# Kernel optimization log

Measured on AMD Instinct MI355X. Metric: run time of the kernel, lower is better.

## Reference

```python
import jax, jax.numpy as jnp
import numpy as np

D_MODEL = 1024
H = 16
DK = D_MODEL // H
D_FC = 4096
B = 2
S = 1024
EPS = 1e-6


def setup_inputs() -> dict:
    key = jax.random.key(0)
    ks = jax.random.split(key, 8)
    sc = 1.0 / np.sqrt(D_MODEL)
    return {
        "x": jax.random.normal(ks[0], (B, S, D_MODEL), dtype=jnp.float32),
        "mask": jnp.ones((B, 1, 1, S), dtype=jnp.int32),
        "w_q": jax.random.normal(ks[1], (D_MODEL, D_MODEL), dtype=jnp.float32) * sc,
        "w_k": jax.random.normal(ks[2], (D_MODEL, D_MODEL), dtype=jnp.float32) * sc,
        "w_v": jax.random.normal(ks[3], (D_MODEL, D_MODEL), dtype=jnp.float32) * sc,
        "w_o": jax.random.normal(ks[4], (D_MODEL, D_MODEL), dtype=jnp.float32) * sc,
        "alpha1": jnp.ones((D_MODEL,), dtype=jnp.float32),
        "beta1": jnp.zeros((D_MODEL,), dtype=jnp.float32),
        "alpha2": jnp.ones((D_MODEL,), dtype=jnp.float32),
        "beta2": jnp.zeros((D_MODEL,), dtype=jnp.float32),
        "fc1_w": jax.random.normal(ks[5], (D_FC, D_MODEL), dtype=jnp.float32) * sc,
        "fc1_b": jnp.zeros((D_FC,), dtype=jnp.float32),
        "fc2_w": jax.random.normal(ks[6], (D_MODEL, D_FC), dtype=jnp.float32) * (1.0 / np.sqrt(D_FC)),
        "fc2_b": jnp.zeros((D_MODEL,), dtype=jnp.float32),
    }


def _layernorm(x, alpha, beta):
    # Matches torch: mean and std (unbiased, ddof=1), divide by (std + eps)
    mean = jnp.mean(x, axis=-1, keepdims=True)
    std = jnp.std(x, axis=-1, keepdims=True, ddof=1)
    return alpha * (x - mean) / (std + EPS) + beta


def _mha(x, mask, w_q, w_k, w_v, w_o):
    # nn.Linear(bias=False): y = x @ W.T
    q = (x @ w_q.T).reshape(B, S, H, DK).transpose(0, 2, 1, 3)  # (B,H,S,DK)
    k = (x @ w_k.T).reshape(B, S, H, DK).transpose(0, 2, 1, 3)
    v = (x @ w_v.T).reshape(B, S, H, DK).transpose(0, 2, 1, 3)
    scores = jnp.einsum('bhqd,bhkd->bhqk', q, k) / jnp.sqrt(jnp.float32(DK))
    scores = jnp.where(mask == 0, jnp.float32(-1e9), scores)
    attn = jax.nn.softmax(scores, axis=-1)  # dropout=0 (eval)
    out = jnp.einsum('bhqk,bhkd->bhqd', attn, v)  # (B,H,S,DK)
    out = out.transpose(0, 2, 1, 3).reshape(B, S, D_MODEL)
    return out @ w_o.T


def _ffn(x, fc1_w, fc1_b, fc2_w, fc2_b):
    h = jax.nn.relu(x @ fc1_w.T + fc1_b)
    return h @ fc2_w.T + fc2_b


def reference(x, mask, w_q, w_k, w_v, w_o, alpha1, beta1, alpha2, beta2,
              fc1_w, fc1_b, fc2_w, fc2_b):
    # Pre-LN residual block 1: attention
    x = x + _mha(_layernorm(x, alpha1, beta1), mask, w_q, w_k, w_v, w_o)
    # Pre-LN residual block 2: FFN
    x = x + _ffn(_layernorm(x, alpha2, beta2), fc1_w, fc1_b, fc2_w, fc2_b)
    return x
```

## Files before the change

kernel.cpp:

```cpp
#include <hip/hip_runtime.h>
#include <hip/hip_bf16.h>


typedef __bf16 bf16;
typedef __attribute__((ext_vector_type(8))) __bf16 bf16x8;
typedef __attribute__((ext_vector_type(4))) __bf16 bf16x4;
typedef __attribute__((ext_vector_type(4))) float f32x4;

#define NTOK 2048
#define DM   1024
#define DFC  4096
#define QKVN 3072

__device__ inline void gl_lds16(const void* g, void* l) {
    __builtin_amdgcn_global_load_lds((const __attribute__((address_space(1))) void*)g,
                                     (__attribute__((address_space(3))) void*)l, 16, 0, 0);
}

__device__ inline void ln_row(float4 v, const float* alpha, const float* beta,
                              bf16* outrow, int t) {
    float s  = v.x + v.y + v.z + v.w;
    float ss = v.x * v.x + v.y * v.y + v.z * v.z + v.w * v.w;
    __shared__ float red[8];
    int lane = t & 63, wv = t >> 6;
    #pragma unroll
    for (int o = 32; o > 0; o >>= 1) {
        s  += __shfl_down(s, o);
        ss += __shfl_down(ss, o);
    }
    if (lane == 0) { red[wv] = s; red[4 + wv] = ss; }
    __syncthreads();
    float S  = red[0] + red[1] + red[2] + red[3];
    float SS = red[4] + red[5] + red[6] + red[7];
    float mean = S * (1.0f / 1024.0f);
    float var  = (SS - S * mean) * (1.0f / 1023.0f);
    var = var < 0.f ? 0.f : var;
    float inv = 1.0f / (sqrtf(var) + 1e-6f);
    float4 a4 = reinterpret_cast<const float4*>(alpha)[t];
    float4 b4 = reinterpret_cast<const float4*>(beta)[t];
    bf16x4 o4;
    o4[0] = (bf16)(a4.x * (v.x - mean) * inv + b4.x);
    o4[1] = (bf16)(a4.y * (v.y - mean) * inv + b4.y);
    o4[2] = (bf16)(a4.z * (v.z - mean) * inv + b4.z);
    o4[3] = (bf16)(a4.w * (v.w - mean) * inv + b4.w);
    reinterpret_cast<bf16x4*>(outrow)[t] = o4;
}

__global__ __launch_bounds__(256) void prep_kernel(
    const float4* __restrict__ wq, const float4* __restrict__ wk,
    const float4* __restrict__ wv, const float4* __restrict__ wo,
    const float4* __restrict__ f1, const float4* __restrict__ f2,
    bf16x4* __restrict__ oqkv, bf16x4* __restrict__ oo,
    bf16x4* __restrict__ of1, bf16x4* __restrict__ of2,
    const float* __restrict__ x, const float* __restrict__ alpha1,
    const float* __restrict__ beta1, bf16* __restrict__ xn) {
    int blk = blockIdx.x;
    int t = threadIdx.x;
    if (blk < 12288) {
        int i = blk * 256 + t;
        const int Q = 262144;
        float4 v;
        bf16x4* dst;
        if (i < 3 * Q) {
            v = (i < Q) ? wq[i] : (i < 2 * Q) ? wk[i - Q] : wv[i - 2 * Q];
            dst = oqkv + i;
        } else if (i < 4 * Q) {
            v = wo[i - 3 * Q];
            dst = oo + (i - 3 * Q);
        } else if (i < 8 * Q) {
            v = f1[i - 4 * Q];
            dst = of1 + (i - 4 * Q);
        } else {
            v = f2[i - 8 * Q];
            dst = of2 + (i - 8 * Q);
        }
        bf16x4 o;
        o[0] = (bf16)v.x; o[1] = (bf16)v.y; o[2] = (bf16)v.z; o[3] = (bf16)v.w;
        *dst = o;
    } else {
        int row = blk - 12288;
        float4 v = reinterpret_cast<const float4*>(x + (size_t)row * DM)[t];
        ln_row(v, alpha1, beta1, xn + (size_t)row * DM, t);
    }
}

__global__ __launch_bounds__(256) void reduce_ln_kernel(const float* __restrict__ p,
                                                        const float* __restrict__ resid,
                                                        const float* __restrict__ alpha,
                                                        const float* __restrict__ beta,
                                                        float* __restrict__ x2,
                                                        bf16* __restrict__ xn) {
    int row = blockIdx.x, t = threadIdx.x;
    size_t i4 = (size_t)row * 256 + t;
    const size_t SL = 524288;
    float4 a = reinterpret_cast<const float4*>(p)[i4];
    float4 b = reinterpret_cast<const float4*>(p)[i4 + SL];
    float4 c = reinterpret_cast<const float4*>(p)[i4 + 2 * SL];
    float4 d = reinterpret_cast<const float4*>(p)[i4 + 3 * SL];
    float4 r = reinterpret_cast<const float4*>(resid)[i4];
    float4 v;
    v.x = a.x + b.x + c.x + d.x + r.x;
    v.y = a.y + b.y + c.y + d.y + r.y;
    v.z = a.z + b.z + c.z + d.z + r.z;
    v.w = a.w + b.w + c.w + d.w + r.w;
    reinterpret_cast<float4*>(x2)[i4] = v;
    ln_row(v, alpha, beta, xn + (size_t)row * DM, t);
}

__global__ __launch_bounds__(256) void reduce_out_kernel(const float* __restrict__ p,
                                                         const float* __restrict__ bias,
                                                         const float* __restrict__ x2,
                                                         float* __restrict__ out) {
    size_t i4 = (size_t)blockIdx.x * 256 + threadIdx.x;
    const size_t SL = 524288;
    float4 a = reinterpret_cast<const float4*>(p)[i4];
    float4 b = reinterpret_cast<const float4*>(p)[i4 + SL];
    float4 c = reinterpret_cast<const float4*>(p)[i4 + 2 * SL];
    float4 d = reinterpret_cast<const float4*>(p)[i4 + 3 * SL];
    float4 r = reinterpret_cast<const float4*>(x2)[i4];
    float4 bi = reinterpret_cast<const float4*>(bias)[i4 & 255];
    float4 o;
    o.x = a.x + b.x + c.x + d.x + r.x + bi.x;
    o.y = a.y + b.y + c.y + d.y + r.y + bi.y;
    o.z = a.z + b.z + c.z + d.z + r.z + bi.z;
    o.w = a.w + b.w + c.w + d.w + r.w + bi.w;
    reinterpret_cast<float4*>(out)[i4] = o;
}

template <int EPI>
__global__ __launch_bounds__(256) void gemm128(const bf16* __restrict__ A,
                                               const bf16* __restrict__ Bt,
                                               void* __restrict__ outp,
                                               bf16* __restrict__ vt,
                                               const float* __restrict__ bias,
                                               int M, int N, int K, int kslice) {
    __shared__ bf16 As[2][128 * 64];
    __shared__ bf16 Bs[2][128 * 64];
    int tid = threadIdx.x;
    int lane = tid & 63, wave = tid >> 6;
    int q = lane >> 4, r = lane & 15;
    int wm = wave >> 1, wn = wave & 1;

    int lid = blockIdx.y * gridDim.x + blockIdx.x;
    int nxp = gridDim.x >> 3;
    int xcd = lid & 7;
    int loc = lid >> 3;
    int bx = xcd * nxp + (loc % nxp);
    int by = loc / nxp;

    int m0 = by * 128, n0 = bx * 128;
    int kbeg = blockIdx.z * kslice;
    int nit = kslice / 64;
    f32x4 acc[4][4] = {};

    int srow = tid >> 3;
    int csrc = (tid & 7) ^ (srow & 7);
    const bf16* agp = A  + (size_t)(m0 + srow) * K + kbeg + csrc * 8;
    const bf16* bgp = Bt + (size_t)(n0 + srow) * K + kbeg + csrc * 8;

    int rsw = (r & 7);
    int co0 = ((q ^ rsw) * 8);
    int co1 = co0 ^ 32;
    int aoff = (wm * 64 + r) * 64;
    int boff = (wn * 64 + r) * 64;

    auto stage = [&](int it, int b) {
        int k0 = it * 64;
        #pragma unroll
        for (int j = 0; j < 4; ++j) {
            gl_lds16(agp + (size_t)j * 32 * K + k0, &As[b][tid * 8 + j * 2048]);
            gl_lds16(bgp + (size_t)j * 32 * K + k0, &Bs[b][tid * 8 + j * 2048]);
        }
    };

    stage(0, 0);
    for (int it = 0; it < nit; ++it) {
        __syncthreads();
        if (it + 1 < nit) stage(it + 1, (it + 1) & 1);
        const bf16* Ab = &As[it & 1][aoff];
        const bf16* Bb = &Bs[it & 1][boff];
        #pragma unroll
        for (int half = 0; half < 2; ++half) {
            int co = half ? co1 : co0;
            bf16x8 af[4], bfv[4];
            #pragma unroll
            for (int t = 0; t < 4; ++t)
                af[t] = *reinterpret_cast<const bf16x8*>(Ab + t * 1024 + co);
            #pragma unroll
            for (int u = 0; u < 4; ++u)
                bfv[u] = *reinterpret_cast<const bf16x8*>(Bb + u * 1024 + co);
            #pragma unroll
            for (int t = 0; t < 4; ++t)
                #pragma unroll
                for (int u = 0; u < 4; ++u)
                    acc[t][u] = __builtin_amdgcn_mfma_f32_16x16x32_bf16(af[t], bfv[u], acc[t][u], 0, 0, 0);
        }
    }

    if (EPI == 2 && n0 >= 2048) {
        int bb = m0 >> 10;
        int sb = (m0 & 1023) + wm * 64 + q * 4;
        int vrow0 = bb * 1024 + (n0 - 2048) + wn * 64;
        #pragma unroll
        for (int t = 0; t < 4; ++t) {
            #pragma unroll
            for (int u = 0; u < 4; ++u) {
                bf16x4 pk;
                #pragma unroll
                for (int i = 0; i < 4; ++i) pk[i] = (bf16)acc[t][u][i];
                *reinterpret_cast<bf16x4*>(vt + (size_t)(vrow0 + u * 16 + r) * 1024 + sb + t * 16) = pk;
            }
        }
        return;
    }

    size_t zoff = (size_t)blockIdx.z * M * N;
    #pragma unroll
    for (int t = 0; t < 4; ++t) {
        #pragma unroll
        for (int u = 0; u < 4; ++u) {
            #pragma unroll
            for (int i = 0; i < 4; ++i) {
                int mm = m0 + wm * 64 + t * 16 + q * 4 + i;
                int nn = n0 + wn * 64 + u * 16 + r;
                size_t idx = (size_t)mm * N + nn;
                float v = acc[t][u][i];
                if (EPI == 0 || EPI == 2) {
                    ((bf16*)outp)[idx] = (bf16)v;
                } else if (EPI == 1) {
                    v += bias[nn];
                    ((bf16*)outp)[idx] = (bf16)(v > 0.f ? v : 0.f);
                } else {
                    ((float*)outp)[zoff + idx] = v;
                }
            }
        }
    }
}

__global__ __launch_bounds__(256) void attn_kernel(const bf16* __restrict__ qkv,
                                                   const bf16* __restrict__ Vt,
                                                   const int* __restrict__ mask,
                                                   bf16* __restrict__ out) {
    __shared__ bf16 Ks[2][4096];
    __shared__ bf16 Vs[2][4096];
    __shared__ bf16 pbuf[4][1024];
    __shared__ float msk[1024];
    int tid = threadIdx.x;
    int lane = tid & 63, w = tid >> 6;
    int q = lane >> 4, r = lane & 15;

    int id = blockIdx.x;
    int xcd = id & 7, j = id >> 3;
    int bh = xcd * 4 + (j >> 4);
    int qb = j & 15;
    int b = bh >> 4, h = bh & 15;

    {
        int4 mi = reinterpret_cast<const int4*>(mask + b * 1024)[tid];
        msk[tid * 4 + 0] = mi.x ? 0.f : -1e9f;
        msk[tid * 4 + 1] = mi.y ? 0.f : -1e9f;
        msk[tid * 4 + 2] = mi.z ? 0.f : -1e9f;
        msk[tid * 4 + 3] = mi.w ? 0.f : -1e9f;
    }

    const bf16* qrow = qkv + (size_t)(b * 1024 + qb * 64 + w * 16 + r) * QKVN + h * 64 + q * 8;
    bf16x8 qf0 = *reinterpret_cast<const bf16x8*>(qrow);
    bf16x8 qf1 = *reinterpret_cast<const bf16x8*>(qrow + 32);

    int csw = (tid & 7) ^ ((tid >> 3) & 7);
    const bf16* kg0 = qkv + (size_t)(b * 1024 + (tid >> 3)) * QKVN + 1024 + h * 64 + csw * 8;
    const bf16* kg1 = kg0 + (size_t)32 * QKVN;
    const bf16* vg0 = Vt + (size_t)((b * 16 + h) * 64 + (tid >> 3)) * 1024 + csw * 8;
    const bf16* vg1 = vg0 + 32 * 1024;
    bf16* kld = &Ks[0][tid * 8];
    bf16* vld = &Vs[0][tid * 8];

    int co0 = (q ^ (r & 7)) * 8;
    bf16* pw = pbuf[w];
    bf16x8 ones;
    #pragma unroll
    for (int jj = 0; jj < 8; ++jj) ones[jj] = (bf16)1.0f;

    float m[4] = {-1e30f, -1e30f, -1e30f, -1e30f};
    f32x4 osum = {};
    f32x4 o[4] = {};

    gl_lds16(kg0, kld);
    gl_lds16(kg1, kld + 2048);
    gl_lds16(vg0, vld);
    gl_lds16(vg1, vld + 2048);

    for (int t = 0; t < 16; ++t) {
        __syncthreads();
        if (t < 15) {
            int ktn = (t + 1) * 64;
            int bo = ((t + 1) & 1) * 4096;
            gl_lds16(kg0 + (size_t)ktn * QKVN, kld + bo);
            gl_lds16(kg1 + (size_t)ktn * QKVN, kld + bo + 2048);
            gl_lds16(vg0 + ktn, vld + bo);
            gl_lds16(vg1 + ktn, vld + bo + 2048);
        }
        const bf16* Kb = Ks[t & 1];
        const bf16* Vb = Vs[t & 1];
        int kt = t * 64;

        f32x4 s[4];
        #pragma unroll
        for (int ks = 0; ks < 4; ++ks) {
            bf16x8 kf0 = *reinterpret_cast<const bf16x8*>(&Kb[(ks * 16 + r) * 64 + co0]);
            bf16x8 kf1 = *reinterpret_cast<const bf16x8*>(&Kb[(ks * 16 + r) * 64 + (co0 ^ 32)]);
            f32x4 a = {};
            a = __builtin_amdgcn_mfma_f32_16x16x32_bf16(qf0, kf0, a, 0, 0, 0);
            a = __builtin_amdgcn_mfma_f32_16x16x32_bf16(qf1, kf1, a, 0, 0, 0);
            float mb = msk[kt + ks * 16 + r];
            #pragma unroll
            for (int i = 0; i < 4; ++i) s[ks][i] = fmaf(a[i], 0.125f, mb);
        }
        float alpha[4];
        #pragma unroll
        for (int i = 0; i < 4; ++i) {
            float t2 = fmaxf(fmaxf(s[0][i], s[1][i]), fmaxf(s[2][i], s[3][i]));
            t2 = fmaxf(t2, __shfl_xor(t2, 1));
            t2 = fmaxf(t2, __shfl_xor(t2, 2));
            t2 = fmaxf(t2, __shfl_xor(t2, 4));
            t2 = fmaxf(t2, __shfl_xor(t2, 8));
            float mn = fmaxf(m[i], t2);
            alpha[i] = __expf(m[i] - mn);
            m[i] = mn;
        }
        #pragma unroll
        for (int i = 0; i < 4; ++i) {
            s[0][i] = __expf(s[0][i] - m[i]);
            s[1][i] = __expf(s[1][i] - m[i]);
            s[2][i] = __expf(s[2][i] - m[i]);
            s[3][i] = __expf(s[3][i] - m[i]);
        }
        #pragma unroll
        for (int i = 0; i < 4; ++i) {
            osum[i] *= alpha[i];
            o[0][i] *= alpha[i]; o[1][i] *= alpha[i];
            o[2][i] *= alpha[i]; o[3][i] *= alpha[i];
        }
        #pragma unroll
        for (int ks = 0; ks < 4; ++ks) {
            int kc = ks * 2 + (r >> 3);
            #pragma unroll
            for (int i = 0; i < 4; ++i) {
                int mr = q * 4 + i;
                pw[mr * 64 + ((kc ^ (mr & 7)) * 8) + (r & 7)] = (bf16)s[ks][i];
            }
        }
        #pragma unroll
        for (int ks2 = 0; ks2 < 2; ++ks2) {
            int vpo = (((ks2 * 4 + q) ^ (r & 7)) * 8);
            bf16x8 pf = *reinterpret_cast<const bf16x8*>(&pw[r * 64 + vpo]);
            #pragma unroll
            for (int nt = 0; nt < 4; ++nt) {
                bf16x8 vf = *reinterpret_cast<const bf16x8*>(&Vb[(nt * 16 + r) * 64 + vpo]);
                o[nt] = __builtin_amdgcn_mfma_f32_16x16x32_bf16(pf, vf, o[nt], 0, 0, 0);
            }
            osum = __builtin_amdgcn_mfma_f32_16x16x32_bf16(pf, ones, osum, 0, 0, 0);
        }
    }

    float inv[4];
    #pragma unroll
    for (int i = 0; i < 4; ++i) inv[i] = 1.0f / osum[i];
    #pragma unroll
    for (int nt = 0; nt < 4; ++nt)
        #pragma unroll
        for (int i = 0; i < 4; ++i)
            out[(size_t)(b * 1024 + qb * 64 + w * 16 + q * 4 + i) * DM + h * 64 + nt * 16 + r] =
                (bf16)(o[nt][i] * inv[i]);
}

extern "C" void kernel_launch(void* const* d_in, const int* in_sizes, int n_in,
                              void* d_out, int out_size, void* d_ws, size_t ws_size,
                              hipStream_t stream) {
    const float* x      = (const float*)d_in[0];
    const int*   mask   = (const int*)  d_in[1];
    const float* w_q    = (const float*)d_in[2];
    const float* w_k    = (const float*)d_in[3];
    const float* w_v    = (const float*)d_in[4];
    const float* w_o    = (const float*)d_in[5];
    const float* alpha1 = (const float*)d_in[6];
    const float* beta1  = (const float*)d_in[7];
    const float* alpha2 = (const float*)d_in[8];
    const float* beta2  = (const float*)d_in[9];
    const float* fc1_w  = (const float*)d_in[10];
    const float* fc1_b  = (const float*)d_in[11];
    const float* fc2_w  = (const float*)d_in[12];
    const float* fc2_b  = (const float*)d_in[13];
    float* out = (float*)d_out;

    char* ws = (char*)d_ws;
    const size_t MB = 1024 * 1024;
    bf16*  wqkv_b = (bf16*)(ws +  0 * MB);
    bf16*  wo_b   = (bf16*)(ws +  6 * MB);
    bf16*  f1w_b  = (bf16*)(ws +  8 * MB);
    bf16*  f2w_b  = (bf16*)(ws + 16 * MB);
    bf16*  xn     = (bf16*)(ws + 24 * MB);
    bf16*  qkvb   = (bf16*)(ws + 28 * MB);
    bf16*  vtb    = (bf16*)(ws + 40 * MB);
    bf16*  attnb  = (bf16*)(ws + 44 * MB);
    float* x2     = (float*)(ws + 48 * MB);
    float* po     = (float*)(ws + 56 * MB);
    bf16*  hb     = (bf16*)(ws + 28 * MB);
    float* pf2    = (float*)(ws + 56 * MB);

    prep_kernel<<<14336, 256, 0, stream>>>(
        (const float4*)w_q, (const float4*)w_k, (const float4*)w_v, (const float4*)w_o,
        (const float4*)fc1_w, (const float4*)fc2_w,
        (bf16x4*)wqkv_b, (bf16x4*)wo_b, (bf16x4*)f1w_b, (bf16x4*)f2w_b,
        x, alpha1, beta1, xn);

    gemm128<2><<<dim3(QKVN / 128, NTOK / 128, 1), 256, 0, stream>>>(
        xn, wqkv_b, qkvb, vtb, nullptr, NTOK, QKVN, DM, DM);

    attn_kernel<<<512, 256, 0, stream>>>(qkvb, vtb, mask, attnb);

    gemm128<4><<<dim3(DM / 128, NTOK / 128, 4), 256, 0, stream>>>(
        attnb, wo_b, po, nullptr, nullptr, NTOK, DM, DM, DM / 4);

    reduce_ln_kernel<<<NTOK, 256, 0, stream>>>(po, x, alpha2, beta2, x2, xn);

    gemm128<1><<<dim3(DFC / 128, NTOK / 128, 1), 256, 0, stream>>>(
        xn, f1w_b, hb, nullptr, fc1_b, NTOK, DFC, DM, DM);

    gemm128<4><<<dim3(DM / 128, NTOK / 128, 4), 256, 0, stream>>>(
        hb, f2w_b, pf2, nullptr, nullptr, NTOK, DM, DFC, DFC / 4);

    reduce_out_kernel<<<2048, 256, 0, stream>>>(pf2, fc2_b, x2, out);
}
```

Measured before the change: 252.2 us.

## Overlap weight conversion with QKV GEMM and replace split-K with 128x64 tiles

```diff
diff --git a/kernel.cpp b/kernel.cpp
--- a/kernel.cpp
+++ b/kernel.cpp
@@ -48,37 +48,20 @@
 
 __global__ __launch_bounds__(256) void prep_kernel(
     const float4* __restrict__ wq, const float4* __restrict__ wk,
-    const float4* __restrict__ wv, const float4* __restrict__ wo,
-    const float4* __restrict__ f1, const float4* __restrict__ f2,
-    bf16x4* __restrict__ oqkv, bf16x4* __restrict__ oo,
-    bf16x4* __restrict__ of1, bf16x4* __restrict__ of2,
+    const float4* __restrict__ wv, bf16x4* __restrict__ oqkv,
     const float* __restrict__ x, const float* __restrict__ alpha1,
     const float* __restrict__ beta1, bf16* __restrict__ xn) {
     int blk = blockIdx.x;
     int t = threadIdx.x;
-    if (blk < 12288) {
+    if (blk < 3072) {
         int i = blk * 256 + t;
         const int Q = 262144;
-        float4 v;
-        bf16x4* dst;
-        if (i < 3 * Q) {
-            v = (i < Q) ? wq[i] : (i < 2 * Q) ? wk[i - Q] : wv[i - 2 * Q];
-            dst = oqkv + i;
-        } else if (i < 4 * Q) {
-            v = wo[i - 3 * Q];
-            dst = oo + (i - 3 * Q);
-        } else if (i < 8 * Q) {
-            v = f1[i - 4 * Q];
-            dst = of1 + (i - 4 * Q);
-        } else {
-            v = f2[i - 8 * Q];
-            dst = of2 + (i - 8 * Q);
-        }
+        float4 v = (i < Q) ? wq[i] : (i < 2 * Q) ? wk[i - Q] : wv[i - 2 * Q];
         bf16x4 o;
         o[0] = (bf16)v.x; o[1] = (bf16)v.y; o[2] = (bf16)v.z; o[3] = (bf16)v.w;
-        *dst = o;
+        oqkv[i] = o;
     } else {
-        int row = blk - 12288;
+        int row = blk - 3072;
         float4 v = reinterpret_cast<const float4*>(x + (size_t)row * DM)[t];
         ln_row(v, alpha1, beta1, xn + (size_t)row * DM, t);
     }
@@ -92,17 +75,10 @@
                                                         bf16* __restrict__ xn) {
     int row = blockIdx.x, t = threadIdx.x;
     size_t i4 = (size_t)row * 256 + t;
-    const size_t SL = 524288;
     float4 a = reinterpret_cast<const float4*>(p)[i4];
-    float4 b = reinterpret_cast<const float4*>(p)[i4 + SL];
-    float4 c = reinterpret_cast<const float4*>(p)[i4 + 2 * SL];
-    float4 d = reinterpret_cast<const float4*>(p)[i4 + 3 * SL];
     float4 r = reinterpret_cast<const float4*>(resid)[i4];
     float4 v;
-    v.x = a.x + b.x + c.x + d.x + r.x;
-    v.y = a.y + b.y + c.y + d.y + r.y;
-    v.z = a.z + b.z + c.z + d.z + r.z;
-    v.w = a.w + b.w + c.w + d.w + r.w;
+    v.x = a.x + r.x; v.y = a.y + r.y; v.z = a.z + r.z; v.w = a.w + r.w;
     reinterpret_cast<float4*>(x2)[i4] = v;
     ln_row(v, alpha, beta, xn + (size_t)row * DM, t);
 }
@@ -112,18 +88,12 @@
                                                          const float* __restrict__ x2,
                                                          float* __restrict__ out) {
     size_t i4 = (size_t)blockIdx.x * 256 + threadIdx.x;
-    const size_t SL = 524288;
     float4 a = reinterpret_cast<const float4*>(p)[i4];
-    float4 b = reinterpret_cast<const float4*>(p)[i4 + SL];
-    float4 c = reinterpret_cast<const float4*>(p)[i4 + 2 * SL];
-    float4 d = reinterpret_cast<const float4*>(p)[i4 + 3 * SL];
     float4 r = reinterpret_cast<const float4*>(x2)[i4];
     float4 bi = reinterpret_cast<const float4*>(bias)[i4 & 255];
     float4 o;
-    o.x = a.x + b.x + c.x + d.x + r.x + bi.x;
-    o.y = a.y + b.y + c.y + d.y + r.y + bi.y;
-    o.z = a.z + b.z + c.z + d.z + r.z + bi.z;
-    o.w = a.w + b.w + c.w + d.w + r.w + bi.w;
+    o.x = a.x + r.x + bi.x; o.y = a.y + r.y + bi.y;
+    o.z = a.z + r.z + bi.z; o.w = a.w + r.w + bi.w;
     reinterpret_cast<float4*>(out)[i4] = o;
 }
 
@@ -133,9 +103,141 @@
                                                void* __restrict__ outp,
                                                bf16* __restrict__ vt,
                                                const float* __restrict__ bias,
-                                               int M, int N, int K, int kslice) {
+                                               int M, int N, int K,
+                                               int nbx, int nby,
+                                               const float4* __restrict__ cwo,
+                                               const float4* __restrict__ cf1,
+                                               const float4* __restrict__ cf2,
+                                               bf16x4* __restrict__ oo,
+                                               bf16x4* __restrict__ of1,
+                                               bf16x4* __restrict__ of2) {
     __shared__ bf16 As[2][128 * 64];
     __shared__ bf16 Bs[2][128 * 64];
+    int tid = threadIdx.x;
+    int lid = blockIdx.y * nbx + blockIdx.x;
+
+    if (EPI == 2) {
+        if (lid >= nbx * nby) {
+            int i = (lid - nbx * nby) * 256 + tid;
+            const int Q = 262144;
+            float4 v;
+            bf16x4* dst;
+            if (i < Q) {
+                v = cwo[i];  dst = oo + i;
+            } else if (i < 5 * Q) {
+                v = cf1[i - Q]; dst = of1 + (i - Q);
+            } else {
+                v = cf2[i - 5 * Q]; dst = of2 + (i - 5 * Q);
+            }
+            bf16x4 o;
+            o[0] = (bf16)v.x; o[1] = (bf16)v.y; o[2] = (bf16)v.z; o[3] = (bf16)v.w;
+            *dst = o;
+            return;
+        }
+    }
+
+    int lane = tid & 63, wave = tid >> 6;
+    int q = lane >> 4, r = lane & 15;
+    int wm = wave >> 1, wn = wave & 1;
+
+    int nxp = nbx >> 3;
+    int xcd = lid & 7;
+    int loc = lid >> 3;
+    int bx = xcd * nxp + (loc % nxp);
+    int by = loc / nxp;
+
+    int m0 = by * 128, n0 = bx * 128;
+    int nit = K / 64;
+    f32x4 acc[4][4] = {};
+
+    int srow = tid >> 3;
+    int csrc = (tid & 7) ^ (srow & 7);
+    const bf16* agp = A  + (size_t)(m0 + srow) * K + csrc * 8;
+    const bf16* bgp = Bt + (size_t)(n0 + srow) * K + csrc * 8;
+
+    int rsw = (r & 7);
+    int co0 = ((q ^ rsw) * 8);
+    int co1 = co0 ^ 32;
+    int aoff = (wm * 64 + r) * 64;
+    int boff = (wn * 64 + r) * 64;
+
+    auto stage = [&](int it, int b) {
+        int k0 = it * 64;
+        #pragma unroll
+        for (int j = 0; j < 4; ++j) {
+            gl_lds16(agp + (size_t)j * 32 * K + k0, &As[b][tid * 8 + j * 2048]);
+            gl_lds16(bgp + (size_t)j * 32 * K + k0, &Bs[b][tid * 8 + j * 2048]);
+        }
+    };
+
+    stage(0, 0);
+    for (int it = 0; it < nit; ++it) {
+        __syncthreads();
+        if (it + 1 < nit) stage(it + 1, (it + 1) & 1);
+        const bf16* Ab = &As[it & 1][aoff];
+        const bf16* Bb = &Bs[it & 1][boff];
+        #pragma unroll
+        for (int half = 0; half < 2; ++half) {
+            int co = half ? co1 : co0;
+            bf16x8 af[4], bfv[4];
+            #pragma unroll
+            for (int t = 0; t < 4; ++t)
+                af[t] = *reinterpret_cast<const bf16x8*>(Ab + t * 1024 + co);
+            #pragma unroll
+            for (int u = 0; u < 4; ++u)
+                bfv[u] = *reinterpret_cast<const bf16x8*>(Bb + u * 1024 + co);
+            #pragma unroll
+            for (int t = 0; t < 4; ++t)
+                #pragma unroll
+                for (int u = 0; u < 4; ++u)
+                    acc[t][u] = __builtin_amdgcn_mfma_f32_16x16x32_bf16(af[t], bfv[u], acc[t][u], 0, 0, 0);
+        }
+    }
+
+    if (EPI == 2 && n0 >= 2048) {
+        int bb = m0 >> 10;
+        int sb = (m0 & 1023) + wm * 64 + q * 4;
+        int vrow0 = bb * 1024 + (n0 - 2048) + wn * 64;
+        #pragma unroll
+        for (int t = 0; t < 4; ++t) {
+            #pragma unroll
+            for (int u = 0; u < 4; ++u) {
+                bf16x4 pk;
+                #pragma unroll
+                for (int i = 0; i < 4; ++i) pk[i] = (bf16)acc[t][u][i];
+                *reinterpret_cast<bf16x4*>(vt + (size_t)(vrow0 + u * 16 + r) * 1024 + sb + t * 16) = pk;
+            }
+        }
+        return;
+    }
+
+    #pragma unroll
+    for (int t = 0; t < 4; ++t) {
+        #pragma unroll
+        for (int u = 0; u < 4; ++u) {
+            #pragma unroll
+            for (int i = 0; i < 4; ++i) {
+                int mm = m0 + wm * 64 + t * 16 + q * 4 + i;
+                int nn = n0 + wn * 64 + u * 16 + r;
+                size_t idx = (size_t)mm * N + nn;
+                float v = acc[t][u][i];
+                if (EPI == 1) {
+                    v += bias[nn];
+                    ((bf16*)outp)[idx] = (bf16)(v > 0.f ? v : 0.f);
+                } else {
+                    ((bf16*)outp)[idx] = (bf16)v;
+                }
+            }
+        }
+    }
+}
+
+__global__ __launch_bounds__(256) void gemm64(const bf16* __restrict__ A,
+                                              const bf16* __restrict__ Bt,
+                                              float* __restrict__ outp,
+                                              int M, int N, int K) {
+    __shared__ bf16 As[2][128 * 64];
+    __shared__ bf16 Bs[2][64 * 64];
     int tid = threadIdx.x;
     int lane = tid & 63, wave = tid >> 6;
     int q = lane >> 4, r = lane & 15;
@@ -148,29 +250,29 @@
     int bx = xcd * nxp + (loc % nxp);
     int by = loc / nxp;
 
-    int m0 = by * 128, n0 = bx * 128;
-    int kbeg = blockIdx.z * kslice;
-    int nit = kslice / 64;
-    f32x4 acc[4][4] = {};
+    int m0 = by * 128, n0 = bx * 64;
+    int nit = K / 64;
+    f32x4 acc[4][2] = {};
 
     int srow = tid >> 3;
     int csrc = (tid & 7) ^ (srow & 7);
-    const bf16* agp = A  + (size_t)(m0 + srow) * K + kbeg + csrc * 8;
-    const bf16* bgp = Bt + (size_t)(n0 + srow) * K + kbeg + csrc * 8;
+    const bf16* agp = A  + (size_t)(m0 + srow) * K + csrc * 8;
+    const bf16* bgp = Bt + (size_t)(n0 + srow) * K + csrc * 8;
 
     int rsw = (r & 7);
     int co0 = ((q ^ rsw) * 8);
     int co1 = co0 ^ 32;
     int aoff = (wm * 64 + r) * 64;
-    int boff = (wn * 64 + r) * 64;
+    int boff = (wn * 32 + r) * 64;
 
     auto stage = [&](int it, int b) {
         int k0 = it * 64;
         #pragma unroll
-        for (int j = 0; j < 4; ++j) {
+        for (int j = 0; j < 4; ++j)
             gl_lds16(agp + (size_t)j * 32 * K + k0, &As[b][tid * 8 + j * 2048]);
+        #pragma unroll
+        for (int j = 0; j < 2; ++j)
             gl_lds16(bgp + (size_t)j * 32 * K + k0, &Bs[b][tid * 8 + j * 2048]);
-        }
     };
 
     stage(0, 0);
@@ -182,57 +284,30 @@
         #pragma unroll
         for (int half = 0; half < 2; ++half) {
             int co = half ? co1 : co0;
-            bf16x8 af[4], bfv[4];
+            bf16x8 af[4], bfv[2];
             #pragma unroll
             for (int t = 0; t < 4; ++t)
                 af[t] = *reinterpret_cast<const bf16x8*>(Ab + t * 1024 + co);
             #pragma unroll
-            for (int u = 0; u < 4; ++u)
+            for (int u = 0; u < 2; ++u)
                 bfv[u] = *reinterpret_cast<const bf16x8*>(Bb + u * 1024 + co);
             #pragma unroll
             for (int t = 0; t < 4; ++t)
                 #pragma unroll
-                for (int u = 0; u < 4; ++u)
+                for (int u = 0; u < 2; ++u)
                     acc[t][u] = __builtin_amdgcn_mfma_f32_16x16x32_bf16(af[t], bfv[u], acc[t][u], 0, 0, 0);
         }
     }
 
-    if (EPI == 2 && n0 >= 2048) {
-        int bb = m0 >> 10;
-        int sb = (m0 & 1023) + wm * 64 + q * 4;
-        int vrow0 = bb * 1024 + (n0 - 2048) + wn * 64;
-        #pragma unroll
-        for (int t = 0; t < 4; ++t) {
-            #pragma unroll
-            for (int u = 0; u < 4; ++u) {
-                bf16x4 pk;
-                #pragma unroll
-                for (int i = 0; i < 4; ++i) pk[i] = (bf16)acc[t][u][i];
-                *reinterpret_cast<bf16x4*>(vt + (size_t)(vrow0 + u * 16 + r) * 1024 + sb + t * 16) = pk;
-            }
-        }
-        return;
-    }
-
-    size_t zoff = (size_t)blockIdx.z * M * N;
     #pragma unroll
     for (int t = 0; t < 4; ++t) {
         #pragma unroll
-        for (int u = 0; u < 4; ++u) {
+        for (int u = 0; u < 2; ++u) {
             #pragma unroll
             for (int i = 0; i < 4; ++i) {
                 int mm = m0 + wm * 64 + t * 16 + q * 4 + i;
-                int nn = n0 + wn * 64 + u * 16 + r;
-                size_t idx = (size_t)mm * N + nn;
-                float v = acc[t][u][i];
-                if (EPI == 0 || EPI == 2) {
-                    ((bf16*)outp)[idx] = (bf16)v;
-                } else if (EPI == 1) {
-                    v += bias[nn];
-                    ((bf16*)outp)[idx] = (bf16)(v > 0.f ? v : 0.f);
-                } else {
-                    ((float*)outp)[zoff + idx] = v;
-                }
+                int nn = n0 + wn * 32 + u * 16 + r;
+                outp[(size_t)mm * N + nn] = acc[t][u][i];
             }
         }
     }
@@ -407,29 +482,30 @@
     float* x2     = (float*)(ws + 48 * MB);
     float* po     = (float*)(ws + 56 * MB);
     bf16*  hb     = (bf16*)(ws + 28 * MB);
-    float* pf2    = (float*)(ws + 56 * MB);
-
-    prep_kernel<<<14336, 256, 0, stream>>>(
-        (const float4*)w_q, (const float4*)w_k, (const float4*)w_v, (const float4*)w_o,
-        (const float4*)fc1_w, (const float4*)fc2_w,
-        (bf16x4*)wqkv_b, (bf16x4*)wo_b, (bf16x4*)f1w_b, (bf16x4*)f2w_b,
-        x, alpha1, beta1, xn);
-
-    gemm128<2><<<dim3(QKVN / 128, NTOK / 128, 1), 256, 0, stream>>>(
-        xn, wqkv_b, qkvb, vtb, nullptr, NTOK, QKVN, DM, DM);
+    float* pf2    = (float*)(ws + 64 * MB);
+
+    prep_kernel<<<5120, 256, 0, stream>>>(
+        (const float4*)w_q, (const float4*)w_k, (const float4*)w_v,
+        (bf16x4*)wqkv_b, x, alpha1, beta1, xn);
+
+    gemm128<2><<<dim3(384 + 9216, 1, 1), 256, 0, stream>>>(
+        xn, wqkv_b, qkvb, vtb, nullptr, NTOK, QKVN, DM, 24, 16,
+        (const float4*)w_o, (const float4*)fc1_w, (const float4*)fc2_w,
+        (bf16x4*)wo_b, (bf16x4*)f1w_b, (bf16x4*)f2w_b);
 
     attn_kernel<<<512, 256, 0, stream>>>(qkvb, vtb, mask, attnb);
 
-    gemm128<4><<<dim3(DM / 128, NTOK / 128, 4), 256, 0, stream>>>(
-        attnb, wo_b, po, nullptr, nullptr, NTOK, DM, DM, DM / 4);
+    gemm64<<<dim3(DM / 64, NTOK / 128, 1), 256, 0, stream>>>(
+        attnb, wo_b, po, NTOK, DM, DM);
 
     reduce_ln_kernel<<<NTOK, 256, 0, stream>>>(po, x, alpha2, beta2, x2, xn);
 
     gemm128<1><<<dim3(DFC / 128, NTOK / 128, 1), 256, 0, stream>>>(
-        xn, f1w_b, hb, nullptr, fc1_b, NTOK, DFC, DM, DM);
-
-    gemm128<4><<<dim3(DM / 128, NTOK / 128, 4), 256, 0, stream>>>(
-        hb, f2w_b, pf2, nullptr, nullptr, NTOK, DM, DFC, DFC / 4);
+        xn, f1w_b, hb, nullptr, fc1_b, NTOK, DFC, DM, 32, 16,
+        nullptr, nullptr, nullptr, nullptr, nullptr, nullptr);
+
+    gemm64<<<dim3(DM / 64, NTOK / 128, 1), 256, 0, stream>>>(
+        hb, f2w_b, pf2, NTOK, DM, DFC);
 
     reduce_out_kernel<<<2048, 256, 0, stream>>>(pf2, fc2_b, x2, out);
 }
```

After: 273.5 us. 8.5% more time.

## Use 8-wave GEMM blocks with triple-buffered LDS and explicit vmcnt waits

Applied to the files above, without the earlier changes.

```diff
diff --git a/kernel.cpp b/kernel.cpp
--- a/kernel.cpp
+++ b/kernel.cpp
@@ -128,21 +128,22 @@
 }
 
 template <int EPI>
-__global__ __launch_bounds__(256) void gemm128(const bf16* __restrict__ A,
+__global__ __launch_bounds__(512) void gemm128(const bf16* __restrict__ A,
                                                const bf16* __restrict__ Bt,
                                                void* __restrict__ outp,
                                                bf16* __restrict__ vt,
                                                const float* __restrict__ bias,
-                                               int M, int N, int K, int kslice) {
-    __shared__ bf16 As[2][128 * 64];
-    __shared__ bf16 Bs[2][128 * 64];
+                                               int M, int N, int K, int kslice,
+                                               int nbx, int nby) {
+    __shared__ bf16 As[3][128 * 64];
+    __shared__ bf16 Bs[3][128 * 64];
     int tid = threadIdx.x;
     int lane = tid & 63, wave = tid >> 6;
     int q = lane >> 4, r = lane & 15;
-    int wm = wave >> 1, wn = wave & 1;
-
-    int lid = blockIdx.y * gridDim.x + blockIdx.x;
-    int nxp = gridDim.x >> 3;
+    int wm = wave >> 2, wn = wave & 3;
+
+    int lid = blockIdx.y * nbx + blockIdx.x;
+    int nxp = nbx >> 3;
     int xcd = lid & 7;
     int loc = lid >> 3;
     int bx = xcd * nxp + (loc % nxp);
@@ -151,60 +152,63 @@
     int m0 = by * 128, n0 = bx * 128;
     int kbeg = blockIdx.z * kslice;
     int nit = kslice / 64;
-    f32x4 acc[4][4] = {};
+    f32x4 acc[4][2] = {};
 
     int srow = tid >> 3;
     int csrc = (tid & 7) ^ (srow & 7);
     const bf16* agp = A  + (size_t)(m0 + srow) * K + kbeg + csrc * 8;
     const bf16* bgp = Bt + (size_t)(n0 + srow) * K + kbeg + csrc * 8;
 
-    int rsw = (r & 7);
-    int co0 = ((q ^ rsw) * 8);
-    int co1 = co0 ^ 32;
+    int co0 = ((q ^ (r & 7)) * 8);
     int aoff = (wm * 64 + r) * 64;
-    int boff = (wn * 64 + r) * 64;
+    int boff = (wn * 32 + r) * 64;
 
     auto stage = [&](int it, int b) {
         int k0 = it * 64;
-        #pragma unroll
-        for (int j = 0; j < 4; ++j) {
-            gl_lds16(agp + (size_t)j * 32 * K + k0, &As[b][tid * 8 + j * 2048]);
-            gl_lds16(bgp + (size_t)j * 32 * K + k0, &Bs[b][tid * 8 + j * 2048]);
-        }
+        gl_lds16(agp + k0,                      &As[b][tid * 8]);
+        gl_lds16(agp + (size_t)64 * K + k0,     &As[b][4096 + tid * 8]);
+        gl_lds16(bgp + k0,                      &Bs[b][tid * 8]);
+        gl_lds16(bgp + (size_t)64 * K + k0,     &Bs[b][4096 + tid * 8]);
     };
 
     stage(0, 0);
+    stage(1, 1);
     for (int it = 0; it < nit; ++it) {
-        __syncthreads();
-        if (it + 1 < nit) stage(it + 1, (it + 1) & 1);
-        const bf16* Ab = &As[it & 1][aoff];
-        const bf16* Bb = &Bs[it & 1][boff];
+        if (it + 1 < nit) asm volatile("s_waitcnt vmcnt(4)" ::: "memory");
+        else              asm volatile("s_waitcnt vmcnt(0)" ::: "memory");
+        __builtin_amdgcn_s_barrier();
+        if (it + 2 < nit) stage(it + 2, (it + 2) % 3);
+
+        const bf16* Ab = &As[it % 3][aoff];
+        const bf16* Bb = &Bs[it % 3][boff];
+        __builtin_amdgcn_s_setprio(1);
         #pragma unroll
         for (int half = 0; half < 2; ++half) {
-            int co = half ? co1 : co0;
-            bf16x8 af[4], bfv[4];
+            int co = co0 ^ (half * 32);
+            bf16x8 af[4], bfv[2];
             #pragma unroll
             for (int t = 0; t < 4; ++t)
                 af[t] = *reinterpret_cast<const bf16x8*>(Ab + t * 1024 + co);
             #pragma unroll
-            for (int u = 0; u < 4; ++u)
+            for (int u = 0; u < 2; ++u)
                 bfv[u] = *reinterpret_cast<const bf16x8*>(Bb + u * 1024 + co);
             #pragma unroll
             for (int t = 0; t < 4; ++t)
                 #pragma unroll
-                for (int u = 0; u < 4; ++u)
+                for (int u = 0; u < 2; ++u)
                     acc[t][u] = __builtin_amdgcn_mfma_f32_16x16x32_bf16(af[t], bfv[u], acc[t][u], 0, 0, 0);
         }
+        __builtin_amdgcn_s_setprio(0);
     }
 
     if (EPI == 2 && n0 >= 2048) {
         int bb = m0 >> 10;
         int sb = (m0 & 1023) + wm * 64 + q * 4;
-        int vrow0 = bb * 1024 + (n0 - 2048) + wn * 64;
+        int vrow0 = bb * 1024 + (n0 - 2048) + wn * 32;
         #pragma unroll
         for (int t = 0; t < 4; ++t) {
             #pragma unroll
-            for (int u = 0; u < 4; ++u) {
+            for (int u = 0; u < 2; ++u) {
                 bf16x4 pk;
                 #pragma unroll
                 for (int i = 0; i < 4; ++i) pk[i] = (bf16)acc[t][u][i];
@@ -218,18 +222,18 @@
     #pragma unroll
     for (int t = 0; t < 4; ++t) {
         #pragma unroll
-        for (int u = 0; u < 4; ++u) {
+        for (int u = 0; u < 2; ++u) {
             #pragma unroll
             for (int i = 0; i < 4; ++i) {
                 int mm = m0 + wm * 64 + t * 16 + q * 4 + i;
-                int nn = n0 + wn * 64 + u * 16 + r;
+                int nn = n0 + wn * 32 + u * 16 + r;
                 size_t idx = (size_t)mm * N + nn;
                 float v = acc[t][u][i];
-                if (EPI == 0 || EPI == 2) {
-                    ((bf16*)outp)[idx] = (bf16)v;
-                } else if (EPI == 1) {
+                if (EPI == 1) {
                     v += bias[nn];
                     ((bf16*)outp)[idx] = (bf16)(v > 0.f ? v : 0.f);
+                } else if (EPI == 2) {
+                    ((bf16*)outp)[idx] = (bf16)v;
                 } else {
                     ((float*)outp)[zoff + idx] = v;
                 }
@@ -415,21 +419,21 @@
         (bf16x4*)wqkv_b, (bf16x4*)wo_b, (bf16x4*)f1w_b, (bf16x4*)f2w_b,
         x, alpha1, beta1, xn);
 
-    gemm128<2><<<dim3(QKVN / 128, NTOK / 128, 1), 256, 0, stream>>>(
-        xn, wqkv_b, qkvb, vtb, nullptr, NTOK, QKVN, DM, DM);
+    gemm128<2><<<dim3(24, 16, 1), 512, 0, stream>>>(
+        xn, wqkv_b, qkvb, vtb, nullptr, NTOK, QKVN, DM, DM, 24, 16);
 
     attn_kernel<<<512, 256, 0, stream>>>(qkvb, vtb, mask, attnb);
 
-    gemm128<4><<<dim3(DM / 128, NTOK / 128, 4), 256, 0, stream>>>(
-        attnb, wo_b, po, nullptr, nullptr, NTOK, DM, DM, DM / 4);
+    gemm128<4><<<dim3(8, 16, 4), 512, 0, stream>>>(
+        attnb, wo_b, po, nullptr, nullptr, NTOK, DM, DM, DM / 4, 8, 16);
 
     reduce_ln_kernel<<<NTOK, 256, 0, stream>>>(po, x, alpha2, beta2, x2, xn);
 
-    gemm128<1><<<dim3(DFC / 128, NTOK / 128, 1), 256, 0, stream>>>(
-        xn, f1w_b, hb, nullptr, fc1_b, NTOK, DFC, DM, DM);
-
-    gemm128<4><<<dim3(DM / 128, NTOK / 128, 4), 256, 0, stream>>>(
-        hb, f2w_b, pf2, nullptr, nullptr, NTOK, DM, DFC, DFC / 4);
+    gemm128<1><<<dim3(32, 16, 1), 512, 0, stream>>>(
+        xn, f1w_b, hb, nullptr, fc1_b, NTOK, DFC, DM, DM, 32, 16);
+
+    gemm128<4><<<dim3(8, 16, 4), 512, 0, stream>>>(
+        hb, f2w_b, pf2, nullptr, nullptr, NTOK, DM, DFC, DFC / 4, 8, 16);
 
     reduce_out_kernel<<<2048, 256, 0, stream>>>(pf2, fc2_b, x2, out);
 }
```

Measured after the change: 295.8 us. +17.3%, slower.

## Rewrite attention with 32x32 MFMA tiles, register-resident P, and lazy rescale

Applied to the files above, without the earlier changes.

```diff
diff --git a/kernel.cpp b/kernel.cpp
--- a/kernel.cpp
+++ b/kernel.cpp
@@ -6,6 +6,8 @@
 typedef __attribute__((ext_vector_type(8))) __bf16 bf16x8;
 typedef __attribute__((ext_vector_type(4))) __bf16 bf16x4;
 typedef __attribute__((ext_vector_type(4))) float f32x4;
+typedef __attribute__((ext_vector_type(16))) float f32x16;
+typedef __attribute__((ext_vector_type(4))) unsigned int u32x4;
 
 #define NTOK 2048
 #define DM   1024
@@ -15,6 +17,12 @@
 __device__ inline void gl_lds16(const void* g, void* l) {
     __builtin_amdgcn_global_load_lds((const __attribute__((address_space(1))) void*)g,
                                      (__attribute__((address_space(3))) void*)l, 16, 0, 0);
+}
+
+__device__ inline unsigned cvtpk_bf16(float lo, float hi) {
+    unsigned r;
+    asm("v_cvt_pk_bf16_f32 %0, %1, %2" : "=v"(r) : "v"(lo), "v"(hi));
+    return r;
 }
 
 __device__ inline void ln_row(float4 v, const float* alpha, const float* beta,
@@ -133,7 +141,8 @@
                                                void* __restrict__ outp,
                                                bf16* __restrict__ vt,
                                                const float* __restrict__ bias,
-                                               int M, int N, int K, int kslice) {
+                                               int M, int N, int K, int kslice,
+                                               int nbx, int nby) {
     __shared__ bf16 As[2][128 * 64];
     __shared__ bf16 Bs[2][128 * 64];
     int tid = threadIdx.x;
@@ -141,8 +150,8 @@
     int q = lane >> 4, r = lane & 15;
     int wm = wave >> 1, wn = wave & 1;
 
-    int lid = blockIdx.y * gridDim.x + blockIdx.x;
-    int nxp = gridDim.x >> 3;
+    int lid = blockIdx.y * nbx + blockIdx.x;
+    int nxp = nbx >> 3;
     int xcd = lid & 7;
     int loc = lid >> 3;
     int bx = xcd * nxp + (loc % nxp);
@@ -158,8 +167,7 @@
     const bf16* agp = A  + (size_t)(m0 + srow) * K + kbeg + csrc * 8;
     const bf16* bgp = Bt + (size_t)(n0 + srow) * K + kbeg + csrc * 8;
 
-    int rsw = (r & 7);
-    int co0 = ((q ^ rsw) * 8);
+    int co0 = ((q ^ (r & 7)) * 8);
     int co1 = co0 ^ 32;
     int aoff = (wm * 64 + r) * 64;
     int boff = (wn * 64 + r) * 64;
@@ -225,11 +233,11 @@
                 int nn = n0 + wn * 64 + u * 16 + r;
                 size_t idx = (size_t)mm * N + nn;
                 float v = acc[t][u][i];
-                if (EPI == 0 || EPI == 2) {
-                    ((bf16*)outp)[idx] = (bf16)v;
-                } else if (EPI == 1) {
+                if (EPI == 1) {
                     v += bias[nn];
                     ((bf16*)outp)[idx] = (bf16)(v > 0.f ? v : 0.f);
+                } else if (EPI == 2) {
+                    ((bf16*)outp)[idx] = (bf16)v;
                 } else {
                     ((float*)outp)[zoff + idx] = v;
                 }
@@ -244,16 +252,16 @@
                                                    bf16* __restrict__ out) {
     __shared__ bf16 Ks[2][4096];
     __shared__ bf16 Vs[2][4096];
-    __shared__ bf16 pbuf[4][1024];
     __shared__ float msk[1024];
+    __shared__ float als[4][32];
     int tid = threadIdx.x;
     int lane = tid & 63, w = tid >> 6;
-    int q = lane >> 4, r = lane & 15;
+    int l5 = lane & 31, hi = lane >> 5;
 
     int id = blockIdx.x;
-    int xcd = id & 7, j = id >> 3;
-    int bh = xcd * 4 + (j >> 4);
-    int qb = j & 15;
+    int xcd = id & 7, jj = id >> 3;
+    int bh = xcd * 4 + (jj >> 3);
+    int qb = jj & 7;
     int b = bh >> 4, h = bh & 15;
 
     {
@@ -264,9 +272,12 @@
         msk[tid * 4 + 3] = mi.w ? 0.f : -1e9f;
     }
 
-    const bf16* qrow = qkv + (size_t)(b * 1024 + qb * 64 + w * 16 + r) * QKVN + h * 64 + q * 8;
-    bf16x8 qf0 = *reinterpret_cast<const bf16x8*>(qrow);
-    bf16x8 qf1 = *reinterpret_cast<const bf16x8*>(qrow + 32);
+    int qrow0 = qb * 128 + w * 32;
+    const bf16* qp = qkv + (size_t)(b * 1024 + qrow0 + l5) * QKVN + h * 64 + hi * 8;
+    bf16x8 qf[4];
+    #pragma unroll
+    for (int ks = 0; ks < 4; ++ks)
+        qf[ks] = *reinterpret_cast<const bf16x8*>(qp + ks * 16);
 
     int csw = (tid & 7) ^ ((tid >> 3) & 7);
     const bf16* kg0 = qkv + (size_t)(b * 1024 + (tid >> 3)) * QKVN + 1024 + h * 64 + csw * 8;
@@ -276,20 +287,14 @@
     bf16* kld = &Ks[0][tid * 8];
     bf16* vld = &Vs[0][tid * 8];
 
-    int co0 = (q ^ (r & 7)) * 8;
-    bf16* pw = pbuf[w];
-    bf16x8 ones;
-    #pragma unroll
-    for (int jj = 0; jj < 8; ++jj) ones[jj] = (bf16)1.0f;
-
-    float m[4] = {-1e30f, -1e30f, -1e30f, -1e30f};
-    f32x4 osum = {};
-    f32x4 o[4] = {};
-
     gl_lds16(kg0, kld);
     gl_lds16(kg1, kld + 2048);
     gl_lds16(vg0, vld);
     gl_lds16(vg1, vld + 2048);
+
+    float m_run = -1e30f, l_half = 0.f;
+    f32x16 o0 = {};
+    f32x16 o1 = {};
 
     for (int t = 0; t < 16; ++t) {
         __syncthreads();
@@ -305,74 +310,104 @@
         const bf16* Vb = Vs[t & 1];
         int kt = t * 64;
 
-        f32x4 s[4];
+        f32x16 s0 = {}, s1 = {};
+        __builtin_amdgcn_s_setprio(1);
         #pragma unroll
         for (int ks = 0; ks < 4; ++ks) {
-            bf16x8 kf0 = *reinterpret_cast<const bf16x8*>(&Kb[(ks * 16 + r) * 64 + co0]);
-            bf16x8 kf1 = *reinterpret_cast<const bf16x8*>(&Kb[(ks * 16 + r) * 64 + (co0 ^ 32)]);
-            f32x4 a = {};
-            a = __builtin_amdgcn_mfma_f32_16x16x32_bf16(qf0, kf0, a, 0, 0, 0);
-            a = __builtin_amdgcn_mfma_f32_16x16x32_bf16(qf1, kf1, a, 0, 0, 0);
-            float mb = msk[kt + ks * 16 + r];
-            #pragma unroll
-            for (int i = 0; i < 4; ++i) s[ks][i] = fmaf(a[i], 0.125f, mb);
-        }
-        float alpha[4];
+            int ch = (((ks << 1) + hi) ^ (l5 & 7)) << 3;
+            bf16x8 k0 = *reinterpret_cast<const bf16x8*>(&Kb[l5 * 64 + ch]);
+            bf16x8 k1 = *reinterpret_cast<const bf16x8*>(&Kb[(32 + l5) * 64 + ch]);
+            s0 = __builtin_amdgcn_mfma_f32_32x32x16_bf16(k0, qf[ks], s0, 0, 0, 0);
+            s1 = __builtin_amdgcn_mfma_f32_32x32x16_bf16(k1, qf[ks], s1, 0, 0, 0);
+        }
+        __builtin_amdgcn_s_setprio(0);
+
+        float p0[16], p1[16];
+        float pmax = -1e30f;
+        #pragma unroll
+        for (int g = 0; g < 4; ++g) {
+            float4 mb0 = *reinterpret_cast<const float4*>(&msk[kt + g * 8 + hi * 4]);
+            float4 mb1 = *reinterpret_cast<const float4*>(&msk[kt + 32 + g * 8 + hi * 4]);
+            #pragma unroll
+            for (int i = 0; i < 4; ++i) {
+                float mbv0 = (i == 0) ? mb0.x : (i == 1) ? mb0.y : (i == 2) ? mb0.z : mb0.w;
+                float mbv1 = (i == 0) ? mb1.x : (i == 1) ? mb1.y : (i == 2) ? mb1.z : mb1.w;
+                float a0 = fmaf(s0[g * 4 + i], 0.125f, mbv0);
+                float a1 = fmaf(s1[g * 4 + i], 0.125f, mbv1);
+                p0[g * 4 + i] = a0;
+                p1[g * 4 + i] = a1;
+                pmax = fmaxf(pmax, fmaxf(a0, a1));
+            }
+        }
+        pmax = fmaxf(pmax, __shfl_xor(pmax, 32));
+        float mnew = fmaxf(m_run, pmax);
+        if (!__all(pmax - m_run <= 8.0f)) {
+            float alpha = __expf(m_run - mnew);
+            m_run = mnew;
+            l_half *= alpha;
+            als[w][l5] = alpha;
+            #pragma unroll
+            for (int g = 0; g < 4; ++g) {
+                float4 av = *reinterpret_cast<const float4*>(&als[w][g * 8 + hi * 4]);
+                o0[g * 4 + 0] *= av.x; o0[g * 4 + 1] *= av.y;
+                o0[g * 4 + 2] *= av.z; o0[g * 4 + 3] *= av.w;
+                o1[g * 4 + 0] *= av.x; o1[g * 4 + 1] *= av.y;
+                o1[g * 4 + 2] *= av.z; o1[g * 4 + 3] *= av.w;
+            }
+        }
+        float sum = 0.f;
+        #pragma unroll
+        for (int rg = 0; rg < 16; ++rg) {
+            p0[rg] = __expf(p0[rg] - m_run);
+            p1[rg] = __expf(p1[rg] - m_run);
+            sum += p0[rg] + p1[rg];
+        }
+        l_half += sum;
+
+        __builtin_amdgcn_s_setprio(1);
+        #pragma unroll
+        for (int tile = 0; tile < 2; ++tile) {
+            const float* pp = tile ? p1 : p0;
+            #pragma unroll
+            for (int kp = 0; kp < 2; ++kp) {
+                unsigned uA0 = cvtpk_bf16(pp[8 * kp + 0], pp[8 * kp + 1]);
+                unsigned uA1 = cvtpk_bf16(pp[8 * kp + 2], pp[8 * kp + 3]);
+                unsigned uB0 = cvtpk_bf16(pp[8 * kp + 4], pp[8 * kp + 5]);
+                unsigned uB1 = cvtpk_bf16(pp[8 * kp + 6], pp[8 * kp + 7]);
+                unsigned us0 = hi ? uB0 : uA0, us1 = hi ? uB1 : uA1;
+                unsigned ug0 = hi ? uA0 : uB0, ug1 = hi ? uA1 : uB1;
+                unsigned r0 = (unsigned)__shfl_xor((int)ug0, 32);
+                unsigned r1 = (unsigned)__shfl_xor((int)ug1, 32);
+                u32x4 pw_;
+                pw_[0] = hi ? r0 : us0;
+                pw_[1] = hi ? r1 : us1;
+                pw_[2] = hi ? us0 : r0;
+                pw_[3] = hi ? us1 : r1;
+                bf16x8 pf = *reinterpret_cast<bf16x8*>(&pw_);
+                int vch = (((tile << 2) + (kp << 1) + hi) ^ (l5 & 7)) << 3;
+                bf16x8 v0 = *reinterpret_cast<const bf16x8*>(&Vb[l5 * 64 + vch]);
+                bf16x8 v1 = *reinterpret_cast<const bf16x8*>(&Vb[(32 + l5) * 64 + vch]);
+                o0 = __builtin_amdgcn_mfma_f32_32x32x16_bf16(pf, v0, o0, 0, 0, 0);
+                o1 = __builtin_amdgcn_mfma_f32_32x32x16_bf16(pf, v1, o1, 0, 0, 0);
+            }
+        }
+        __builtin_amdgcn_s_setprio(0);
+    }
+
+    float l_tot = l_half + __shfl_xor(l_half, 32);
+    als[w][l5] = 1.0f / l_tot;
+    bf16* ob = out + (size_t)(b * 1024 + qrow0) * DM + h * 64;
+    #pragma unroll
+    for (int g = 0; g < 4; ++g) {
+        float4 iv = *reinterpret_cast<const float4*>(&als[w][g * 8 + hi * 4]);
         #pragma unroll
         for (int i = 0; i < 4; ++i) {
-            float t2 = fmaxf(fmaxf(s[0][i], s[1][i]), fmaxf(s[2][i], s[3][i]));
-            t2 = fmaxf(t2, __shfl_xor(t2, 1));
-            t2 = fmaxf(t2, __shfl_xor(t2, 2));
-            t2 = fmaxf(t2, __shfl_xor(t2, 4));
-            t2 = fmaxf(t2, __shfl_xor(t2, 8));
-            float mn = fmaxf(m[i], t2);
-            alpha[i] = __expf(m[i] - mn);
-            m[i] = mn;
-        }
-        #pragma unroll
-        for (int i = 0; i < 4; ++i) {
-            s[0][i] = __expf(s[0][i] - m[i]);
-            s[1][i] = __expf(s[1][i] - m[i]);
-            s[2][i] = __expf(s[2][i] - m[i]);
-            s[3][i] = __expf(s[3][i] - m[i]);
-        }
-        #pragma unroll
-        for (int i = 0; i < 4; ++i) {
-            osum[i] *= alpha[i];
-            o[0][i] *= alpha[i]; o[1][i] *= alpha[i];
-            o[2][i] *= alpha[i]; o[3][i] *= alpha[i];
-        }
-        #pragma unroll
-        for (int ks = 0; ks < 4; ++ks) {
-            int kc = ks * 2 + (r >> 3);
-            #pragma unroll
-            for (int i = 0; i < 4; ++i) {
-                int mr = q * 4 + i;
-                pw[mr * 64 + ((kc ^ (mr & 7)) * 8) + (r & 7)] = (bf16)s[ks][i];
-            }
-        }
-        #pragma unroll
-        for (int ks2 = 0; ks2 < 2; ++ks2) {
-            int vpo = (((ks2 * 4 + q) ^ (r & 7)) * 8);
-            bf16x8 pf = *reinterpret_cast<const bf16x8*>(&pw[r * 64 + vpo]);
-            #pragma unroll
-            for (int nt = 0; nt < 4; ++nt) {
-                bf16x8 vf = *reinterpret_cast<const bf16x8*>(&Vb[(nt * 16 + r) * 64 + vpo]);
-                o[nt] = __builtin_amdgcn_mfma_f32_16x16x32_bf16(pf, vf, o[nt], 0, 0, 0);
-            }
-            osum = __builtin_amdgcn_mfma_f32_16x16x32_bf16(pf, ones, osum, 0, 0, 0);
-        }
-    }
-
-    float inv[4];
-    #pragma unroll
-    for (int i = 0; i < 4; ++i) inv[i] = 1.0f / osum[i];
-    #pragma unroll
-    for (int nt = 0; nt < 4; ++nt)
-        #pragma unroll
-        for (int i = 0; i < 4; ++i)
-            out[(size_t)(b * 1024 + qb * 64 + w * 16 + q * 4 + i) * DM + h * 64 + nt * 16 + r] =
-                (bf16)(o[nt][i] * inv[i]);
+            float ivv = (i == 0) ? iv.x : (i == 1) ? iv.y : (i == 2) ? iv.z : iv.w;
+            int qr = g * 8 + hi * 4 + i;
+            ob[(size_t)qr * DM + l5]      = (bf16)(o0[g * 4 + i] * ivv);
+            ob[(size_t)qr * DM + 32 + l5] = (bf16)(o1[g * 4 + i] * ivv);
+        }
+    }
 }
 
 extern "C" void kernel_launch(void* const* d_in, const int* in_sizes, int n_in,
@@ -415,21 +450,21 @@
         (bf16x4*)wqkv_b, (bf16x4*)wo_b, (bf16x4*)f1w_b, (bf16x4*)f2w_b,
         x, alpha1, beta1, xn);
 
-    gemm128<2><<<dim3(QKVN / 128, NTOK / 128, 1), 256, 0, stream>>>(
-        xn, wqkv_b, qkvb, vtb, nullptr, NTOK, QKVN, DM, DM);
-
-    attn_kernel<<<512, 256, 0, stream>>>(qkvb, vtb, mask, attnb);
-
-    gemm128<4><<<dim3(DM / 128, NTOK / 128, 4), 256, 0, stream>>>(
-        attnb, wo_b, po, nullptr, nullptr, NTOK, DM, DM, DM / 4);
+    gemm128<2><<<dim3(24, 16, 1), 256, 0, stream>>>(
+        xn, wqkv_b, qkvb, vtb, nullptr, NTOK, QKVN, DM, DM, 24, 16);
+
+    attn_kernel<<<256, 256, 0, stream>>>(qkvb, vtb, mask, attnb);
+
+    gemm128<4><<<dim3(8, 16, 4), 256, 0, stream>>>(
+        attnb, wo_b, po, nullptr, nullptr, NTOK, DM, DM, DM / 4, 8, 16);
 
     reduce_ln_kernel<<<NTOK, 256, 0, stream>>>(po, x, alpha2, beta2, x2, xn);
 
-    gemm128<1><<<dim3(DFC / 128, NTOK / 128, 1), 256, 0, stream>>>(
-        xn, f1w_b, hb, nullptr, fc1_b, NTOK, DFC, DM, DM);
-
-    gemm128<4><<<dim3(DM / 128, NTOK / 128, 4), 256, 0, stream>>>(
-        hb, f2w_b, pf2, nullptr, nullptr, NTOK, DM, DFC, DFC / 4);
+    gemm128<1><<<dim3(32, 16, 1), 256, 0, stream>>>(
+        xn, f1w_b, hb, nullptr, fc1_b, NTOK, DFC, DM, DM, 32, 16);
+
+    gemm128<4><<<dim3(8, 16, 4), 256, 0, stream>>>(
+        hb, f2w_b, pf2, nullptr, nullptr, NTOK, DM, DFC, DFC / 4, 8, 16);
 
     reduce_out_kernel<<<2048, 256, 0, stream>>>(pf2, fc2_b, x2, out);
 }
```

After: 246.4 us. 2.3% less time.
